# Kernel optimization log

Measured on AMD Instinct MI355X. Metric: run time of the kernel, lower is better.

Reference implementation:

```python
import jax, jax.numpy as jnp
import numpy as np
from jax import lax

INV_SQRT2 = np.float32(1.0 / np.sqrt(2.0))

def conv2d(x, w, b=None, stride=1, pad=0):
    y = lax.conv_general_dilated(x, w, (stride, stride), [(pad, pad), (pad, pad)],
                                 dimension_numbers=('NCHW', 'OIHW', 'NCHW'))
    return y if b is None else y + b[None, :, None, None]

def haar_dwt2_zero(x):
    # pytorch_wavelets DWTForward(J=1, wave='haar', mode='zero') for odd H,W:
    # pad one zero at the end of each spatial dim, then pairwise Haar analysis.
    x = jnp.pad(x, ((0, 0), (0, 0), (0, 1), (0, 1)))
    xe, xo = x[..., 0::2], x[..., 1::2]
    lo_w, hi_w = (xe + xo) * INV_SQRT2, (xe - xo) * INV_SQRT2
    def rows(t):
        te, to = t[:, :, 0::2, :], t[:, :, 1::2, :]
        return (te + to) * INV_SQRT2, (te - to) * INV_SQRT2
    ll, lh = rows(lo_w)
    hl, hh = rows(hi_w)
    return ll, lh, hl, hh  # cA, cH, cV, cD

def pixel_shuffle2(x):
    B, C, H, W = x.shape
    co = C // 4
    return x.reshape(B, co, 2, 2, H, W).transpose(0, 1, 4, 2, 5, 3).reshape(B, co, H * 2, W * 2)

def gaussian_kernel5(sigma=0.5):
    r = np.arange(5, dtype=np.float64) - 2.0
    k = np.exp(-(r ** 2) / (2.0 * sigma * sigma))
    return jnp.asarray((k / k.sum()).astype(np.float32))

_GK = gaussian_kernel5(0.5)

def gaussian_blur5(x4d):
    # cv2.GaussianBlur ksize=(5,5) sigma=0.5, default BORDER_REFLECT_101 -> 'reflect' pad
    p = jnp.pad(x4d, ((0, 0), (0, 0), (2, 2), (2, 2)), mode='reflect')
    p = conv2d(p, _GK.reshape(1, 1, 5, 1))
    return conv2d(p, _GK.reshape(1, 1, 1, 5))

def channel_attention(x, w1, w2):
    avg = jnp.mean(x, axis=(2, 3), keepdims=True)
    mx = jnp.max(x, axis=(2, 3), keepdims=True)
    mlp = lambda v: conv2d(jax.nn.relu(conv2d(v, w1)), w2)
    return jax.nn.sigmoid(mlp(avg) + mlp(mx)) * x

def _forward(x, w_x1, b_x1, w_x2, b_x2, w_x3, b_x3, w_hi, b_hi, w_lo, b_lo,
             ca1_w1, ca1_w2, ca2_w1, ca2_w2, w_cat, b_cat, w_c9a, b_c9a, w_c9b, b_c9b):
    f1 = jax.nn.relu(conv2d(x, w_x1, b_x1))            # (1,16,H,W)
    f2 = jax.nn.relu(conv2d(f1, w_x2, b_x2))           # (1,8,H,W)
    tmp12 = jax.nn.relu(conv2d(f2, w_x3, b_x3))        # (1,1,H,W)
    cA, cH, cV, cD = haar_dwt2_zero(tmp12)             # each (1,1,(H+1)/2,(W+1)/2)
    hf = pixel_shuffle2(jax.nn.relu(conv2d(jnp.concatenate([cH, cV, cD], 1), w_hi, b_hi, pad=1)))
    lf = pixel_shuffle2(jax.nn.relu(conv2d(cA, w_lo, b_lo, pad=1)))  # (1,1,H+5,W+5)
    # original detaches hf (cpu->numpy->cv2->cuda): gradients do not flow through it
    hf = gaussian_blur5(lax.stop_gradient(hf))
    hf = channel_attention(hf, ca1_w1, ca1_w2)
    lf = channel_attention(lf, ca2_w1, ca2_w2)
    alpha = 1.0
    cat = jax.nn.relu(conv2d(jnp.concatenate([alpha * hf, (1.0 - alpha) * lf], 1), w_cat, b_cat))
    f12 = tmp12 + cat                                   # (1,1,H,W)
    h = jax.nn.relu(conv2d(f12, w_c9a, b_c9a, pad=1))   # (1,32,H,W)
    return jax.nn.relu(conv2d(h, w_c9b, b_c9b, pad=1))  # (1,64,H,W)

def setup_inputs() -> dict:
    key = jax.random.key(0)
    ks = jax.random.split(key, 24)
    f32 = jnp.float32
    n = lambda k, s, sc=0.05: jax.random.normal(k, s, f32) * sc
    H = W = 511
    return {
        'x': jax.random.normal(ks[0], (1, 204, H, W), f32),
        'w_x1': n(ks[1], (16, 204, 1, 1)), 'b_x1': n(ks[2], (16,)),
        'w_x2': n(ks[3], (8, 16, 1, 1)),   'b_x2': n(ks[4], (8,)),
        'w_x3': n(ks[5], (1, 8, 1, 1)),    'b_x3': n(ks[6], (1,)),
        'w_hi': n(ks[7], (4, 3, 1, 1)),    'b_hi': n(ks[8], (4,)),
        'w_lo': n(ks[9], (4, 1, 1, 1)),    'b_lo': n(ks[10], (4,)),
        'ca1_w1': n(ks[11], (1, 1, 1, 1), 0.5), 'ca1_w2': n(ks[12], (1, 1, 1, 1), 0.5),
        'ca2_w1': n(ks[13], (1, 1, 1, 1), 0.5), 'ca2_w2': n(ks[14], (1, 1, 1, 1), 0.5),
        'w_cat': n(ks[15], (1, 2, 6, 6)),  'b_cat': n(ks[16], (1,)),
        'w_c9a': n(ks[17], (32, 1, 3, 3)), 'b_c9a': n(ks[18], (32,)),
        'w_c9b': n(ks[19], (64, 32, 3, 3)), 'b_c9b': n(ks[20], (64,)),
    }

def reference(x, w_x1, b_x1, w_x2, b_x2, w_x3, b_x3, w_hi, b_hi, w_lo, b_lo,
              ca1_w1, ca1_w2, ca2_w1, ca2_w2, w_cat, b_cat, w_c9a, b_c9a, w_c9b, b_c9b):
    return _forward(x, w_x1, b_x1, w_x2, b_x2, w_x3, b_x3, w_hi, b_hi, w_lo, b_lo,
                    ca1_w1, ca1_w2, ca2_w1, ca2_w2, w_cat, b_cat, w_c9a, b_c9a, w_c9b, b_c9b)
```

## Files before the change

### kernel.cpp

```cpp
#include <hip/hip_runtime.h>
#include <hip/hip_bf16.h>
#include <math.h>

#define NP    261121
#define SPB   512
#define RS    520
#define OFS   16640
#define WPX   520
#define ROWN  4160
#define PSTR  2138240
#define NBLUR 1041

typedef __attribute__((ext_vector_type(8))) short short8;
typedef __attribute__((ext_vector_type(4))) short short4v;
typedef __attribute__((ext_vector_type(4))) float f32x4;
typedef __attribute__((ext_vector_type(4), aligned(4))) float f32x4a;

static __device__ __forceinline__ unsigned short f2bf(float f) {
    unsigned int u = __builtin_bit_cast(unsigned int, f);
    u += 0x7FFFu + ((u >> 16) & 1u);
    return (unsigned short)(u >> 16);
}

static __device__ __forceinline__ short bf16s(float f) {
    __hip_bfloat16 h = __float2bfloat16(f);
    return __builtin_bit_cast(short, h);
}

__global__ __launch_bounds__(256, 2) void k_conv123(const float* __restrict__ x,
                                                    const float* __restrict__ w_x1,
                                                    const float* __restrict__ b1,
                                                    const float* __restrict__ w2,
                                                    const float* __restrict__ b2,
                                                    const float* __restrict__ w3,
                                                    const float* __restrict__ b3,
                                                    float* __restrict__ tmp12)
{
    __shared__ unsigned short sb[2 * OFS];

    const int tid = threadIdx.x;
    const int v = tid >> 6, l = tid & 63;
    const int lpx = l & 15, kg = l >> 4;
    int pxb = blockIdx.x * SPB;
    if (pxb > NP - SPB) pxb = NP - SPB;

    short8 afr[7];
    {
        const float* wrow = w_x1 + lpx * 204;
#pragma unroll
        for (int ks = 0; ks < 7; ++ks)
#pragma unroll
            for (int j = 0; j < 8; ++j) {
                int c = ks * 32 + kg * 8 + j;
                afr[ks][j] = (short)f2bf(c < 204 ? wrow[c] : 0.f);
            }
    }

    const float* xb = x + pxb + 4 * l;
    const float* lpB[8];
#pragma unroll
    for (int i = 0; i < 8; ++i)
        lpB[i] = xb + (size_t)(v * 8 + i) * NP;

    f32x4 acc[8];
#pragma unroll
    for (int n = 0; n < 8; ++n) acc[n] = (f32x4){0.f, 0.f, 0.f, 0.f};

    f32x4a q0[8], q1[8];

#define LOADISSUE(KS) do { \
        _Pragma("unroll") \
        for (int i = 0; i < 8; ++i) { \
            const float* p = ((KS) < 6 || v * 8 + i < 12) ? lpB[i] + (size_t)(KS) * 32 * NP : xb; \
            q0[i] = *reinterpret_cast<const f32x4a*>(p); \
            q1[i] = *reinterpret_cast<const f32x4a*>(p + 256); \
        } \
    } while (0)

#define CVTWRITE(BUF) do { \
        _Pragma("unroll") \
        for (int i = 0; i < 8; ++i) { \
            unsigned short* row = sb + (BUF) * OFS + (v * 8 + i) * RS; \
            short4v w0, w1; \
            _Pragma("unroll") \
            for (int n = 0; n < 4; ++n) { w0[n] = bf16s(q0[i][n]); w1[n] = bf16s(q1[i][n]); } \
            *reinterpret_cast<short4v*>(row + 4 * l)       = w0; \
            *reinterpret_cast<short4v*>(row + 256 + 4 * l) = w1; \
        } \
    } while (0)

#define COMPUTE(KS, BUF) do { \
        short8 r0, r1, r2, r3, r4, r5, r6, r7; \
        const unsigned short* base = sb + (BUF) * OFS + kg * 8 * RS + v * 128 + lpx * 8; \
        r0 = *reinterpret_cast<const short8*>(base); \
        r1 = *reinterpret_cast<const short8*>(base + RS); \
        r2 = *reinterpret_cast<const short8*>(base + 2 * RS); \
        r3 = *reinterpret_cast<const short8*>(base + 3 * RS); \
        r4 = *reinterpret_cast<const short8*>(base + 4 * RS); \
        r5 = *reinterpret_cast<const short8*>(base + 5 * RS); \
        r6 = *reinterpret_cast<const short8*>(base + 6 * RS); \
        r7 = *reinterpret_cast<const short8*>(base + 7 * RS); \
        _Pragma("unroll") \
        for (int n = 0; n < 8; ++n) { \
            short8 b; \
            b[0] = r0[n]; b[1] = r1[n]; b[2] = r2[n]; b[3] = r3[n]; \
            b[4] = r4[n]; b[5] = r5[n]; b[6] = r6[n]; b[7] = r7[n]; \
            acc[n] = __builtin_amdgcn_mfma_f32_16x16x32_bf16(afr[KS], b, acc[n], 0, 0, 0); \
        } \
    } while (0)

    LOADISSUE(0);
    CVTWRITE(0);

#define STEP(K, LAST) do { \
        __syncthreads(); \
        if (!(LAST)) LOADISSUE((K) + 1); \
        COMPUTE((K), (K) & 1); \
        if (!(LAST)) CVTWRITE(((K) + 1) & 1); \
    } while (0)

    STEP(0, 0); STEP(1, 0); STEP(2, 0); STEP(3, 0); STEP(4, 0); STEP(5, 0); STEP(6, 1);
#undef LOADISSUE
#undef CVTWRITE
#undef COMPUTE
#undef STEP

    float4 b1v = *reinterpret_cast<const float4*>(b1 + kg * 4);
    float4 w2v[8];
#pragma unroll
    for (int j = 0; j < 8; ++j)
        w2v[j] = *reinterpret_cast<const float4*>(w2 + j * 16 + kg * 4);
    float b2v[8], w3v[8];
#pragma unroll
    for (int j = 0; j < 8; ++j) { b2v[j] = b2[j]; w3v[j] = w3[j]; }
    float b3v = b3[0];

    f32x4 rlo, rhi;
#pragma unroll
    for (int n = 0; n < 8; ++n) {
        float f0 = fmaxf(acc[n][0] + b1v.x, 0.f);
        float f1 = fmaxf(acc[n][1] + b1v.y, 0.f);
        float f2 = fmaxf(acc[n][2] + b1v.z, 0.f);
        float f3 = fmaxf(acc[n][3] + b1v.w, 0.f);
        float tmp = b3v;
#pragma unroll
        for (int j = 0; j < 8; ++j) {
            float sj = f0 * w2v[j].x;
            sj = fmaf(f1, w2v[j].y, sj);
            sj = fmaf(f2, w2v[j].z, sj);
            sj = fmaf(f3, w2v[j].w, sj);
            sj += __shfl_xor(sj, 16, 64);
            sj += __shfl_xor(sj, 32, 64);
            tmp = fmaf(fmaxf(sj + b2v[j], 0.f), w3v[j], tmp);
        }
        if (n < 4) rlo[n] = fmaxf(tmp, 0.f);
        else       rhi[n - 4] = fmaxf(tmp, 0.f);
    }
    if (kg == 0) {
        float* dst = tmp12 + pxb + v * 128 + lpx * 8;
        *reinterpret_cast<f32x4a*>(dst)     = rlo;
        *reinterpret_cast<f32x4a*>(dst + 4) = rhi;
    }
}

__global__ __launch_bounds__(256) void k_dwt(const float* __restrict__ tmp12,
                                             const float* __restrict__ w_hi,
                                             const float* __restrict__ b_hi,
                                             const float* __restrict__ w_c9b,
                                             float* __restrict__ hf,
                                             unsigned short* __restrict__ wb2,
                                             unsigned short* __restrict__ h2)
{
    int t = blockIdx.x * 256 + threadIdx.x;

    if (t < 18432) {
        int o = t / 288, ck = t - o * 288;
        int c = ck / 9, k = ck - c * 9;
        wb2[k * 2048 + o * 32 + c] = f2bf(w_c9b[t]);
    }
    short8 z8 = {0, 0, 0, 0, 0, 0, 0, 0};
    if (t < 4160) {
        int pl = t / 1040;
        int rr = t - pl * 1040;
        int row = rr >= 520 ? 512 : 0;
        int ch  = rr >= 520 ? rr - 520 : rr;
        *reinterpret_cast<short8*>(h2 + (size_t)pl * PSTR + (size_t)row * ROWN + ch * 8) = z8;
    }
    int z = t - 4160;
    if (z >= 0 && z < 6132) {
        int row = z / 12 + 1;
        int j = z - (row - 1) * 12;
        int pl = j / 3, cidx = j - pl * 3;
        int col = (cidx == 0) ? 0 : (cidx == 1 ? 512 : 513);
        *reinterpret_cast<short8*>(h2 + (size_t)pl * PSTR + (size_t)row * ROWN + col * 8) = z8;
    }

    const float INV = 0.70710678118654752440f;
    if (t >= 258 * 258) return;
    int h = t / 258, w = t - h * 258;

    float wh[12], bh[4];
#pragma unroll
    for (int i = 0; i < 12; ++i) wh[i] = w_hi[i];
#pragma unroll
    for (int o = 0; o < 4; ++o) bh[o] = b_hi[o];

    float v[4];
    if (h == 0 || h == 257 || w == 0 || w == 257) {
#pragma unroll
        for (int o = 0; o < 4; ++o) v[o] = fmaxf(bh[o], 0.f);
    } else {
        int hh = h - 1, ww = w - 1;
        int r0 = 2 * hh, r1 = 2 * hh + 1, c0 = 2 * ww, c1 = 2 * ww + 1;
        float a = tmp12[r0 * 511 + c0];
        float b = (c1 < 511) ? tmp12[r0 * 511 + c1] : 0.f;
        float c = (r1 < 511) ? tmp12[r1 * 511 + c0] : 0.f;
        float d = (r1 < 511 && c1 < 511) ? tmp12[r1 * 511 + c1] : 0.f;
        float lo0 = (a + b) * INV, hi0 = (a - b) * INV;
        float lo1 = (c + d) * INV, hi1 = (c - d) * INV;
        float cH = (lo0 - lo1) * INV;
        float cV = (hi0 + hi1) * INV;
        float cD = (hi0 - hi1) * INV;
#pragma unroll
        for (int o = 0; o < 4; ++o)
            v[o] = fmaxf(wh[o * 3 + 0] * cH + wh[o * 3 + 1] * cV + wh[o * 3 + 2] * cD + bh[o], 0.f);
    }
    int orow = (2 * h) * 516 + 2 * w;
    hf[orow]       = v[0];
    hf[orow + 1]   = v[1];
    hf[orow + 516] = v[2];
    hf[orow + 517] = v[3];
}

__global__ __launch_bounds__(256) void k_blur(const float* __restrict__ hf,
                                              float* __restrict__ hfb,
                                              float* __restrict__ psum,
                                              float* __restrict__ pmax,
                                              float g0, float g1, float g2)
{
    __shared__ float ss[256], sm[256];
    int t = threadIdx.x;
    int idx = blockIdx.x * 256 + t;
    bool ok = idx < 516 * 516;
    int idc = ok ? idx : 0;
    int y = idc / 516, x = idc - y * 516;
    float g[5] = {g0, g1, g2, g1, g0};
    int ry[5], rx[5];
#pragma unroll
    for (int i = 0; i < 5; ++i) {
        int yy = y + i - 2; yy = yy < 0 ? -yy : (yy > 515 ? 1030 - yy : yy);
        int xx = x + i - 2; xx = xx < 0 ? -xx : (xx > 515 ? 1030 - xx : xx);
        ry[i] = yy * 516; rx[i] = xx;
    }
    float s = 0.f;
#pragma unroll
    for (int i = 0; i < 5; ++i) {
        float rs = 0.f;
#pragma unroll
        for (int j = 0; j < 5; ++j) rs = fmaf(g[j], hf[ry[i] + rx[j]], rs);
        s = fmaf(g[i], rs, s);
    }
    if (ok) hfb[idx] = s;

    ss[t] = ok ? s : 0.f;
    sm[t] = ok ? s : -3.4e38f;
    __syncthreads();
    for (int off = 128; off > 0; off >>= 1) {
        if (t < off) { ss[t] += ss[t + off]; sm[t] = fmaxf(sm[t], sm[t + off]); }
        __syncthreads();
    }
    if (t == 0) { psum[blockIdx.x] = ss[0]; pmax[blockIdx.x] = sm[0]; }
}

__global__ __launch_bounds__(256) void k_cat(const float* __restrict__ hfb,
                                             const float* __restrict__ tmp12,
                                             const float* __restrict__ psum,
                                             const float* __restrict__ pmax,
                                             const float* __restrict__ caw1,
                                             const float* __restrict__ caw2,
                                             const float* __restrict__ w_cat,
                                             const float* __restrict__ b_cat,
                                             float* __restrict__ f12)
{
    __shared__ float ss[256], sm[256], ssc;
    int t = threadIdx.x;
    {
        float s = 0.f, m = -3.4e38f;
        for (int i = t; i < NBLUR; i += 256) { s += psum[i]; m = fmaxf(m, pmax[i]); }
        ss[t] = s; sm[t] = m;
        __syncthreads();
        for (int off = 128; off > 0; off >>= 1) {
            if (t < off) { ss[t] += ss[t + off]; sm[t] = fmaxf(sm[t], sm[t + off]); }
            __syncthreads();
        }
        if (t == 0) {
            float avg = ss[0] / 266256.f;
            float a = caw1[0], b = caw2[0];
            float z = b * fmaxf(a * avg, 0.f) + b * fmaxf(a * sm[0], 0.f);
            ssc = 1.f / (1.f + expf(-z));
        }
        __syncthreads();
    }
    float sc = ssc;

    int p = blockIdx.x * 256 + t;
    if (p >= NP) return;
    int y = p / 511, x = p - y * 511;
    float s = 0.f;
#pragma unroll
    for (int ky = 0; ky < 6; ++ky) {
        const float* row = hfb + (y + ky) * 516 + x;
#pragma unroll
        for (int kx = 0; kx < 6; ++kx) s = fmaf(row[kx], w_cat[ky * 6 + kx], s);
    }
    f12[p] = tmp12[p] + fmaxf(sc * s + b_cat[0], 0.f);
}

__global__ __launch_bounds__(256) void k_c9a(const float* __restrict__ f12,
                                             const float* __restrict__ w_c9a,
                                             const float* __restrict__ bias,
                                             unsigned short* __restrict__ h2)
{
    int p = blockIdx.x * 256 + threadIdx.x;
    if (p >= NP) return;
    int y = p / 511, x = p - y * 511;
    float hv[9];
#pragma unroll
    for (int ky = 0; ky < 3; ++ky)
#pragma unroll
        for (int kx = 0; kx < 3; ++kx) {
            int yy = y + ky - 1, xx = x + kx - 1;
            hv[ky * 3 + kx] = (yy >= 0 && yy < 511 && xx >= 0 && xx < 511) ? f12[yy * 511 + xx] : 0.f;
        }
    float acc[32];
#pragma unroll
    for (int o = 0; o < 32; ++o) acc[o] = bias[o];
#pragma unroll
    for (int k = 0; k < 9; ++k) {
        float v = hv[k];
#pragma unroll
        for (int o = 0; o < 32; ++o) acc[o] = fmaf(v, w_c9a[o * 9 + k], acc[o]);
    }
    unsigned short o16[32];
#pragma unroll
    for (int o = 0; o < 32; ++o) o16[o] = f2bf(fmaxf(acc[o], 0.f));
    size_t px = (size_t)(y + 1) * WPX + (x + 1);
#pragma unroll
    for (int i = 0; i < 4; ++i)
        *reinterpret_cast<short8*>(h2 + (size_t)i * PSTR + px * 8) =
            reinterpret_cast<const short8*>(o16)[i];
}

__global__ __launch_bounds__(256, 3) void k_c9b(const unsigned short* __restrict__ h2,
                                                const unsigned short* __restrict__ wb2,
                                                const float* __restrict__ bias,
                                                float* __restrict__ out)
{
    __shared__ unsigned short swu[9 * 2048];

    int bid = blockIdx.x;
    int xcd = bid & 7, jj = bid >> 3;
    const int q = 127, r = 6;
    int wg = (xcd < r ? xcd * (q + 1) : r * (q + 1) + (xcd - r) * q) + jj;

    int lane = threadIdx.x & 63;
    int wave = threadIdx.x >> 6;
    int y  = wg >> 1;
    int xh = wg & 1;
    int xb = xh * 256 + wave * 64;
    int lpx = lane & 15, kg = lane >> 4;

    {
        const short8* wsrc = reinterpret_cast<const short8*>(wb2);
        short8* wdst = reinterpret_cast<short8*>(swu);
        for (int d = threadIdx.x; d < 2304; d += 256) {
            int kt = d >> 8, rem = d & 255, m = rem >> 6, l = rem & 63;
            wdst[d] = wsrc[kt * 256 + (m * 16 + (l & 15)) * 4 + (l >> 4)];
        }
    }
    __syncthreads();

    f32x4 acc[4][4];
#pragma unroll
    for (int m = 0; m < 4; ++m)
#pragma unroll
        for (int n = 0; n < 4; ++n) acc[m][n] = (f32x4){0.f, 0.f, 0.f, 0.f};

    const unsigned short* hb = h2 + (size_t)kg * PSTR;
    const int base_px = (y + 1) * WPX + (xb + 1) + lpx;
    const int rowm = base_px - WPX, row0 = base_px, rowp = base_px + WPX;
    const short8* swv = reinterpret_cast<const short8*>(swu);

#define LOADB(BUF, ROW, DX) do { \
        const unsigned short* rp = hb + (size_t)((ROW) + (DX)) * 8; \
        BUF[0] = *reinterpret_cast<const short8*>(rp); \
        BUF[1] = *reinterpret_cast<const short8*>(rp + 128); \
        BUF[2] = *reinterpret_cast<const short8*>(rp + 256); \
        BUF[3] = *reinterpret_cast<const short8*>(rp + 384); \
    } while (0)

#define TAP(KT, BUF) do { \
        const short8* ap = swv + (KT) * 256 + lane; \
        short8 a0 = ap[0], a1 = ap[64], a2 = ap[128], a3 = ap[192]; \
        _Pragma("unroll") \
        for (int n = 0; n < 4; ++n) { \
            acc[0][n] = __builtin_amdgcn_mfma_f32_16x16x32_bf16(a0, BUF[n], acc[0][n], 0, 0, 0); \
            acc[1][n] = __builtin_amdgcn_mfma_f32_16x16x32_bf16(a1, BUF[n], acc[1][n], 0, 0, 0); \
            acc[2][n] = __builtin_amdgcn_mfma_f32_16x16x32_bf16(a2, BUF[n], acc[2][n], 0, 0, 0); \
            acc[3][n] = __builtin_amdgcn_mfma_f32_16x16x32_bf16(a3, BUF[n], acc[3][n], 0, 0, 0); \
        } \
    } while (0)

    short8 bX[4], bY[4], bZ[4];
    LOADB(bX, rowm, -1);
    LOADB(bY, rowm,  0);
    LOADB(bZ, rowm, +1); TAP(0, bX);
    LOADB(bX, row0, -1); TAP(1, bY);
    LOADB(bY, row0,  0); TAP(2, bZ);
    LOADB(bZ, row0, +1); TAP(3, bX);
    LOADB(bX, rowp, -1); TAP(4, bY);
    LOADB(bY, rowp,  0); TAP(5, bZ);
    LOADB(bZ, rowp, +1); TAP(6, bX);
    TAP(7, bY);
    TAP(8, bZ);
#undef LOADB
#undef TAP

    const int ybase = y * 511;
#pragma unroll
    for (int m = 0; m < 4; ++m) {
#pragma unroll
        for (int rr = 0; rr < 4; ++rr) {
            int o = m * 16 + kg * 4 + rr;
            float bo = bias[o];
#pragma unroll
            for (int n = 0; n < 4; ++n) {
                int px = xb + n * 16 + lpx;
                if (px < 511)
                    out[(size_t)o * NP + ybase + px] = fmaxf(acc[m][n][rr] + bo, 0.f);
            }
        }
    }
}

extern "C" void kernel_launch(void* const* d_in, const int* in_sizes, int n_in,
                              void* d_out, int out_size, void* d_ws, size_t ws_size,
                              hipStream_t stream)
{
    (void)in_sizes; (void)n_in; (void)out_size; (void)ws_size;

    const float* x     = (const float*)d_in[0];
    const float* w_x1  = (const float*)d_in[1];
    const float* b_x1  = (const float*)d_in[2];
    const float* w_x2  = (const float*)d_in[3];
    const float* b_x2  = (const float*)d_in[4];
    const float* w_x3  = (const float*)d_in[5];
    const float* b_x3  = (const float*)d_in[6];
    const float* w_hi  = (const float*)d_in[7];
    const float* b_hi  = (const float*)d_in[8];
    const float* ca1w1 = (const float*)d_in[11];
    const float* ca1w2 = (const float*)d_in[12];
    const float* w_cat = (const float*)d_in[15];
    const float* b_cat = (const float*)d_in[16];
    const float* w_c9a = (const float*)d_in[17];
    const float* b_c9a = (const float*)d_in[18];
    const float* w_c9b = (const float*)d_in[19];
    const float* b_c9b = (const float*)d_in[20];

    float* ws    = (float*)d_ws;
    float* tmp12 = ws + 0;
    float* hf    = ws + 261184;
    float* hfb   = ws + 527488;
    float* f12   = ws + 793792;
    float* psum  = ws + 1054976;
    float* pmax  = ws + 1056032;
    unsigned short* wb2 = (unsigned short*)(ws + 1057088);
    unsigned short* h2  = (unsigned short*)(ws + 1066304);

    float* out = (float*)d_out;

    double kk[5], ssum = 0.0;
    for (int i = 0; i < 5; ++i) { double r = i - 2.0; kk[i] = exp(-r * r / 0.5); ssum += kk[i]; }
    float g0 = (float)(kk[0] / ssum), g1 = (float)(kk[1] / ssum), g2 = (float)(kk[2] / ssum);

    k_conv123<<<511, 256, 0, stream>>>(x, w_x1, b_x1, w_x2, b_x2, w_x3, b_x3, tmp12);
    k_dwt<<<261, 256, 0, stream>>>(tmp12, w_hi, b_hi, w_c9b, hf, wb2, h2);
    k_blur<<<NBLUR, 256, 0, stream>>>(hf, hfb, psum, pmax, g0, g1, g2);
    k_cat<<<1021, 256, 0, stream>>>(hfb, tmp12, psum, pmax, ca1w1, ca1w2, w_cat, b_cat, f12);
    k_c9a<<<1021, 256, 0, stream>>>(f12, w_c9a, b_c9a, h2);
    k_c9b<<<1022, 256, 0, stream>>>(h2, wb2, b_c9b, out);
}
```

Measured before the change: 113.7 us.

## Fuse DWT with blur and cat with c9a, move prep into conv123

The DWT and Gaussian blur are merged into one tiled kernel that builds each 32x32 tile plus halo in shared memory, so the intermediate hf buffer is never written to global memory. The cat conv and the c9a conv are merged the same way with an 18x18 f12 tile in shared memory, so f12 no longer goes through global memory. The weight conversion and h2 border zeroing move into conv123, and the next-stage load is issued before the barrier there. Together this removes two kernel launches and two global round trips, at the cost of recomputing halo cells and some redundant 6x6 work at tile edges.

Result: faster. 103.4 us (median of 2 runs) (-9.1%).

```diff
diff --git a/kernel.cpp b/kernel.cpp
--- a/kernel.cpp
+++ b/kernel.cpp
@@ -9,7 +9,7 @@
 #define WPX   520
 #define ROWN  4160
 #define PSTR  2138240
-#define NBLUR 1041
+#define NBP   289
 
 typedef __attribute__((ext_vector_type(8))) short short8;
 typedef __attribute__((ext_vector_type(4))) short short4v;
@@ -34,8 +34,36 @@
                                                     const float* __restrict__ b2,
                                                     const float* __restrict__ w3,
                                                     const float* __restrict__ b3,
-                                                    float* __restrict__ tmp12)
+                                                    const float* __restrict__ w_c9b,
+                                                    float* __restrict__ tmp12,
+                                                    unsigned short* __restrict__ wb2,
+                                                    unsigned short* __restrict__ h2)
 {
+    {
+        int t = blockIdx.x * 256 + threadIdx.x;
+        if (t < 18432) {
+            int o = t / 288, ck = t - o * 288;
+            int c = ck / 9, k = ck - c * 9;
+            wb2[k * 2048 + o * 32 + c] = f2bf(w_c9b[t]);
+        }
+        short8 z8 = {0, 0, 0, 0, 0, 0, 0, 0};
+        if (t < 4160) {
+            int pl = t / 1040;
+            int rr = t - pl * 1040;
+            int row = rr >= 520 ? 512 : 0;
+            int ch  = rr >= 520 ? rr - 520 : rr;
+            *reinterpret_cast<short8*>(h2 + (size_t)pl * PSTR + (size_t)row * ROWN + ch * 8) = z8;
+        }
+        int z = t - 4160;
+        if (z >= 0 && z < 6132) {
+            int row = z / 12 + 1;
+            int j = z - (row - 1) * 12;
+            int pl = j / 3, cidx = j - pl * 3;
+            int col = (cidx == 0) ? 0 : (cidx == 1 ? 512 : 513);
+            *reinterpret_cast<short8*>(h2 + (size_t)pl * PSTR + (size_t)row * ROWN + col * 8) = z8;
+        }
+    }
+
     __shared__ unsigned short sb[2 * OFS];
 
     const int tid = threadIdx.x;
@@ -113,8 +141,8 @@
     CVTWRITE(0);
 
 #define STEP(K, LAST) do { \
+        if (!(LAST)) LOADISSUE((K) + 1); \
         __syncthreads(); \
-        if (!(LAST)) LOADISSUE((K) + 1); \
         COMPUTE((K), (K) & 1); \
         if (!(LAST)) CVTWRITE(((K) + 1) & 1); \
     } while (0)
@@ -163,41 +191,28 @@
     }
 }
 
-__global__ __launch_bounds__(256) void k_dwt(const float* __restrict__ tmp12,
-                                             const float* __restrict__ w_hi,
-                                             const float* __restrict__ b_hi,
-                                             const float* __restrict__ w_c9b,
-                                             float* __restrict__ hf,
-                                             unsigned short* __restrict__ wb2,
-                                             unsigned short* __restrict__ h2)
+__global__ __launch_bounds__(256) void k_dwtblur(const float* __restrict__ tmp12,
+                                                 const float* __restrict__ w_hi,
+                                                 const float* __restrict__ b_hi,
+                                                 float* __restrict__ hfb,
+                                                 float* __restrict__ psum,
+                                                 float* __restrict__ pmax,
+                                                 float g0, float g1, float g2)
 {
-    int t = blockIdx.x * 256 + threadIdx.x;
-
-    if (t < 18432) {
-        int o = t / 288, ck = t - o * 288;
-        int c = ck / 9, k = ck - c * 9;
-        wb2[k * 2048 + o * 32 + c] = f2bf(w_c9b[t]);
-    }
-    short8 z8 = {0, 0, 0, 0, 0, 0, 0, 0};
-    if (t < 4160) {
-        int pl = t / 1040;
-        int rr = t - pl * 1040;
-        int row = rr >= 520 ? 512 : 0;
-        int ch  = rr >= 520 ? rr - 520 : rr;
-        *reinterpret_cast<short8*>(h2 + (size_t)pl * PSTR + (size_t)row * ROWN + ch * 8) = z8;
-    }
-    int z = t - 4160;
-    if (z >= 0 && z < 6132) {
-        int row = z / 12 + 1;
-        int j = z - (row - 1) * 12;
-        int pl = j / 3, cidx = j - pl * 3;
-        int col = (cidx == 0) ? 0 : (cidx == 1 ? 512 : 513);
-        *reinterpret_cast<short8*>(h2 + (size_t)pl * PSTR + (size_t)row * ROWN + col * 8) = z8;
-    }
-
+    __shared__ float hfT[36][37];
+    __shared__ float ss[256], sm[256];
     const float INV = 0.70710678118654752440f;
-    if (t >= 258 * 258) return;
-    int h = t / 258, w = t - h * 258;
+
+    int tid = threadIdx.x;
+    int bx = blockIdx.x % 17, by = blockIdx.x / 17;
+    int X0 = bx * 32, Y0 = by * 32;
+    int Ylo = Y0 - 2 < 0 ? 0 : Y0 - 2;
+    int Yhi = Y0 + 33 > 515 ? 515 : Y0 + 33;
+    int Xlo = X0 - 2 < 0 ? 0 : X0 - 2;
+    int Xhi = X0 + 33 > 515 ? 515 : X0 + 33;
+    int hlo = Ylo >> 1, hhi = Yhi >> 1, nh = hhi - hlo + 1;
+    int wlo = Xlo >> 1, whi = Xhi >> 1, nw = whi - wlo + 1;
+    int ncells = nh * nw;
 
     float wh[12], bh[4];
 #pragma unroll
@@ -205,95 +220,103 @@
 #pragma unroll
     for (int o = 0; o < 4; ++o) bh[o] = b_hi[o];
 
-    float v[4];
-    if (h == 0 || h == 257 || w == 0 || w == 257) {
-#pragma unroll
-        for (int o = 0; o < 4; ++o) v[o] = fmaxf(bh[o], 0.f);
-    } else {
-        int hh = h - 1, ww = w - 1;
-        int r0 = 2 * hh, r1 = 2 * hh + 1, c0 = 2 * ww, c1 = 2 * ww + 1;
-        float a = tmp12[r0 * 511 + c0];
-        float b = (c1 < 511) ? tmp12[r0 * 511 + c1] : 0.f;
-        float c = (r1 < 511) ? tmp12[r1 * 511 + c0] : 0.f;
-        float d = (r1 < 511 && c1 < 511) ? tmp12[r1 * 511 + c1] : 0.f;
-        float lo0 = (a + b) * INV, hi0 = (a - b) * INV;
-        float lo1 = (c + d) * INV, hi1 = (c - d) * INV;
-        float cH = (lo0 - lo1) * INV;
-        float cV = (hi0 + hi1) * INV;
-        float cD = (hi0 - hi1) * INV;
-#pragma unroll
-        for (int o = 0; o < 4; ++o)
-            v[o] = fmaxf(wh[o * 3 + 0] * cH + wh[o * 3 + 1] * cV + wh[o * 3 + 2] * cD + bh[o], 0.f);
-    }
-    int orow = (2 * h) * 516 + 2 * w;
-    hf[orow]       = v[0];
-    hf[orow + 1]   = v[1];
-    hf[orow + 516] = v[2];
-    hf[orow + 517] = v[3];
-}
-
-__global__ __launch_bounds__(256) void k_blur(const float* __restrict__ hf,
-                                              float* __restrict__ hfb,
-                                              float* __restrict__ psum,
-                                              float* __restrict__ pmax,
-                                              float g0, float g1, float g2)
-{
-    __shared__ float ss[256], sm[256];
-    int t = threadIdx.x;
-    int idx = blockIdx.x * 256 + t;
-    bool ok = idx < 516 * 516;
-    int idc = ok ? idx : 0;
-    int y = idc / 516, x = idc - y * 516;
+    for (int ci = tid; ci < ncells; ci += 256) {
+        int h = hlo + ci / nw, w = wlo + ci % nw;
+        float v[4];
+        if (h == 0 || h == 257 || w == 0 || w == 257) {
+#pragma unroll
+            for (int o = 0; o < 4; ++o) v[o] = fmaxf(bh[o], 0.f);
+        } else {
+            int hh = h - 1, ww = w - 1;
+            int r0 = 2 * hh, r1 = 2 * hh + 1, c0 = 2 * ww, c1 = 2 * ww + 1;
+            float a = tmp12[r0 * 511 + c0];
+            float b = (c1 < 511) ? tmp12[r0 * 511 + c1] : 0.f;
+            float c = (r1 < 511) ? tmp12[r1 * 511 + c0] : 0.f;
+            float d = (r1 < 511 && c1 < 511) ? tmp12[r1 * 511 + c1] : 0.f;
+            float lo0 = (a + b) * INV, hi0 = (a - b) * INV;
+            float lo1 = (c + d) * INV, hi1 = (c - d) * INV;
+            float cH = (lo0 - lo1) * INV;
+            float cV = (hi0 + hi1) * INV;
+            float cD = (hi0 - hi1) * INV;
+#pragma unroll
+            for (int o = 0; o < 4; ++o)
+                v[o] = fmaxf(wh[o * 3 + 0] * cH + wh[o * 3 + 1] * cV + wh[o * 3 + 2] * cD + bh[o], 0.f);
+        }
+#pragma unroll
+        for (int dy = 0; dy < 2; ++dy)
+#pragma unroll
+            for (int dx = 0; dx < 2; ++dx) {
+                int Y = 2 * h + dy, X = 2 * w + dx;
+                if (Y >= Ylo && Y <= Yhi && X >= Xlo && X <= Xhi)
+                    hfT[Y - Y0 + 2][X - X0 + 2] = v[dy * 2 + dx];
+            }
+    }
+    __syncthreads();
+
     float g[5] = {g0, g1, g2, g1, g0};
-    int ry[5], rx[5];
-#pragma unroll
-    for (int i = 0; i < 5; ++i) {
-        int yy = y + i - 2; yy = yy < 0 ? -yy : (yy > 515 ? 1030 - yy : yy);
-        int xx = x + i - 2; xx = xx < 0 ? -xx : (xx > 515 ? 1030 - xx : xx);
-        ry[i] = yy * 516; rx[i] = xx;
-    }
-    float s = 0.f;
-#pragma unroll
-    for (int i = 0; i < 5; ++i) {
-        float rs = 0.f;
-#pragma unroll
-        for (int j = 0; j < 5; ++j) rs = fmaf(g[j], hf[ry[i] + rx[j]], rs);
-        s = fmaf(g[i], rs, s);
-    }
-    if (ok) hfb[idx] = s;
-
-    ss[t] = ok ? s : 0.f;
-    sm[t] = ok ? s : -3.4e38f;
+    float lsum = 0.f, lmax = -3.4e38f;
+#pragma unroll
+    for (int k2 = 0; k2 < 4; ++k2) {
+        int o = tid + k2 * 256;
+        int oy = o >> 5, ox = o & 31;
+        int gy = Y0 + oy, gx = X0 + ox;
+        if (gy < 516 && gx < 516) {
+            int ly[5], lx[5];
+#pragma unroll
+            for (int i = 0; i < 5; ++i) {
+                int yy = gy + i - 2; yy = yy < 0 ? -yy : (yy > 515 ? 1030 - yy : yy);
+                int xx = gx + i - 2; xx = xx < 0 ? -xx : (xx > 515 ? 1030 - xx : xx);
+                ly[i] = yy - Y0 + 2; lx[i] = xx - X0 + 2;
+            }
+            float s = 0.f;
+#pragma unroll
+            for (int i = 0; i < 5; ++i) {
+                float rs = 0.f;
+#pragma unroll
+                for (int j = 0; j < 5; ++j) rs = fmaf(g[j], hfT[ly[i]][lx[j]], rs);
+                s = fmaf(g[i], rs, s);
+            }
+            hfb[gy * 516 + gx] = s;
+            lsum += s; lmax = fmaxf(lmax, s);
+        }
+    }
+
+    ss[tid] = lsum; sm[tid] = lmax;
     __syncthreads();
     for (int off = 128; off > 0; off >>= 1) {
-        if (t < off) { ss[t] += ss[t + off]; sm[t] = fmaxf(sm[t], sm[t + off]); }
+        if (tid < off) { ss[tid] += ss[tid + off]; sm[tid] = fmaxf(sm[tid], sm[tid + off]); }
         __syncthreads();
     }
-    if (t == 0) { psum[blockIdx.x] = ss[0]; pmax[blockIdx.x] = sm[0]; }
-}
-
-__global__ __launch_bounds__(256) void k_cat(const float* __restrict__ hfb,
-                                             const float* __restrict__ tmp12,
-                                             const float* __restrict__ psum,
-                                             const float* __restrict__ pmax,
-                                             const float* __restrict__ caw1,
-                                             const float* __restrict__ caw2,
-                                             const float* __restrict__ w_cat,
-                                             const float* __restrict__ b_cat,
-                                             float* __restrict__ f12)
+    if (tid == 0) { psum[blockIdx.x] = ss[0]; pmax[blockIdx.x] = sm[0]; }
+}
+
+__global__ __launch_bounds__(256) void k_catc9a(const float* __restrict__ hfb,
+                                                const float* __restrict__ tmp12,
+                                                const float* __restrict__ psum,
+                                                const float* __restrict__ pmax,
+                                                const float* __restrict__ caw1,
+                                                const float* __restrict__ caw2,
+                                                const float* __restrict__ w_cat,
+                                                const float* __restrict__ b_cat,
+                                                const float* __restrict__ w_c9a,
+                                                const float* __restrict__ bias9a,
+                                                unsigned short* __restrict__ h2)
 {
-    __shared__ float ss[256], sm[256], ssc;
-    int t = threadIdx.x;
+    __shared__ float f12T[18][19];
+    __shared__ float ss[256], sm[256];
+    __shared__ float ssc;
+    int tid = threadIdx.x;
+
     {
         float s = 0.f, m = -3.4e38f;
-        for (int i = t; i < NBLUR; i += 256) { s += psum[i]; m = fmaxf(m, pmax[i]); }
-        ss[t] = s; sm[t] = m;
+        for (int i = tid; i < NBP; i += 256) { s += psum[i]; m = fmaxf(m, pmax[i]); }
+        ss[tid] = s; sm[tid] = m;
         __syncthreads();
         for (int off = 128; off > 0; off >>= 1) {
-            if (t < off) { ss[t] += ss[t + off]; sm[t] = fmaxf(sm[t], sm[t + off]); }
+            if (tid < off) { ss[tid] += ss[tid + off]; sm[tid] = fmaxf(sm[tid], sm[tid + off]); }
             __syncthreads();
         }
-        if (t == 0) {
+        if (tid == 0) {
             float avg = ss[0] / 266256.f;
             float a = caw1[0], b = caw2[0];
             float z = b * fmaxf(a * avg, 0.f) + b * fmaxf(a * sm[0], 0.f);
@@ -303,38 +326,40 @@
     }
     float sc = ssc;
 
-    int p = blockIdx.x * 256 + t;
-    if (p >= NP) return;
-    int y = p / 511, x = p - y * 511;
-    float s = 0.f;
-#pragma unroll
-    for (int ky = 0; ky < 6; ++ky) {
-        const float* row = hfb + (y + ky) * 516 + x;
-#pragma unroll
-        for (int kx = 0; kx < 6; ++kx) s = fmaf(row[kx], w_cat[ky * 6 + kx], s);
-    }
-    f12[p] = tmp12[p] + fmaxf(sc * s + b_cat[0], 0.f);
-}
-
-__global__ __launch_bounds__(256) void k_c9a(const float* __restrict__ f12,
-                                             const float* __restrict__ w_c9a,
-                                             const float* __restrict__ bias,
-                                             unsigned short* __restrict__ h2)
-{
-    int p = blockIdx.x * 256 + threadIdx.x;
-    if (p >= NP) return;
-    int y = p / 511, x = p - y * 511;
+    int tx0 = (blockIdx.x & 31) * 16, ty0 = (blockIdx.x >> 5) * 16;
+
+    for (int idx = tid; idx < 324; idx += 256) {
+        int r = idx / 18, c = idx - 18 * r;
+        int fy = ty0 - 1 + r, fx = tx0 - 1 + c;
+        float val = 0.f;
+        if (fy >= 0 && fy < 511 && fx >= 0 && fx < 511) {
+            float a6 = 0.f;
+#pragma unroll
+            for (int ky = 0; ky < 6; ++ky) {
+                const float* row = hfb + (fy + ky) * 516 + fx;
+#pragma unroll
+                for (int kx = 0; kx < 6; ++kx) a6 = fmaf(row[kx], w_cat[ky * 6 + kx], a6);
+            }
+            val = tmp12[fy * 511 + fx] + fmaxf(sc * a6 + b_cat[0], 0.f);
+        }
+        f12T[r][c] = val;
+    }
+    __syncthreads();
+
+    int lr = tid >> 4, lc = tid & 15;
+    int oy = ty0 + lr, ox = tx0 + lc;
+    if (oy >= 511 || ox >= 511) return;
+
     float hv[9];
 #pragma unroll
     for (int ky = 0; ky < 3; ++ky)
 #pragma unroll
-        for (int kx = 0; kx < 3; ++kx) {
-            int yy = y + ky - 1, xx = x + kx - 1;
-            hv[ky * 3 + kx] = (yy >= 0 && yy < 511 && xx >= 0 && xx < 511) ? f12[yy * 511 + xx] : 0.f;
-        }
+        for (int kx = 0; kx < 3; ++kx)
+            hv[ky * 3 + kx] = f12T[lr + ky][lc + kx];
+
     float acc[32];
 #pragma unroll
-    for (int o = 0; o < 32; ++o) acc[o] = bias[o];
+    for (int o = 0; o < 32; ++o) acc[o] = bias9a[o];
 #pragma unroll
     for (int k = 0; k < 9; ++k) {
         float v = hv[k];
@@ -344,7 +369,7 @@
     unsigned short o16[32];
 #pragma unroll
     for (int o = 0; o < 32; ++o) o16[o] = f2bf(fmaxf(acc[o], 0.f));
-    size_t px = (size_t)(y + 1) * WPX + (x + 1);
+    size_t px = (size_t)(oy + 1) * WPX + (ox + 1);
 #pragma unroll
     for (int i = 0; i < 4; ++i)
         *reinterpret_cast<short8*>(h2 + (size_t)i * PSTR + px * 8) =
@@ -469,13 +494,11 @@
 
     float* ws    = (float*)d_ws;
     float* tmp12 = ws + 0;
-    float* hf    = ws + 261184;
-    float* hfb   = ws + 527488;
-    float* f12   = ws + 793792;
-    float* psum  = ws + 1054976;
-    float* pmax  = ws + 1056032;
-    unsigned short* wb2 = (unsigned short*)(ws + 1057088);
-    unsigned short* h2  = (unsigned short*)(ws + 1066304);
+    float* hfb   = ws + 261184;
+    float* psum  = ws + 527488;
+    float* pmax  = ws + 527808;
+    unsigned short* wb2 = (unsigned short*)(ws + 528128);
+    unsigned short* h2  = (unsigned short*)(ws + 537344);
 
     float* out = (float*)d_out;
 
@@ -483,10 +506,10 @@
     for (int i = 0; i < 5; ++i) { double r = i - 2.0; kk[i] = exp(-r * r / 0.5); ssum += kk[i]; }
     float g0 = (float)(kk[0] / ssum), g1 = (float)(kk[1] / ssum), g2 = (float)(kk[2] / ssum);
 
-    k_conv123<<<511, 256, 0, stream>>>(x, w_x1, b_x1, w_x2, b_x2, w_x3, b_x3, tmp12);
-    k_dwt<<<261, 256, 0, stream>>>(tmp12, w_hi, b_hi, w_c9b, hf, wb2, h2);
-    k_blur<<<NBLUR, 256, 0, stream>>>(hf, hfb, psum, pmax, g0, g1, g2);
-    k_cat<<<1021, 256, 0, stream>>>(hfb, tmp12, psum, pmax, ca1w1, ca1w2, w_cat, b_cat, f12);
-    k_c9a<<<1021, 256, 0, stream>>>(f12, w_c9a, b_c9a, h2);
+    k_conv123<<<511, 256, 0, stream>>>(x, w_x1, b_x1, w_x2, b_x2, w_x3, b_x3, w_c9b,
+                                       tmp12, wb2, h2);
+    k_dwtblur<<<NBP, 256, 0, stream>>>(tmp12, w_hi, b_hi, hfb, psum, pmax, g0, g1, g2);
+    k_catc9a<<<1024, 256, 0, stream>>>(hfb, tmp12, psum, pmax, ca1w1, ca1w2,
+                                       w_cat, b_cat, w_c9a, b_c9a, h2);
     k_c9b<<<1022, 256, 0, stream>>>(h2, wb2, b_c9b, out);
 }
```
